# Optimization experiments

Measured on AMD Instinct MI355X. Metric: run time of the kernel, lower is better.

The kernel has to match this reference:

```python
import jax, jax.numpy as jnp
import numpy as np

NUM_CLASSES = 2
KS = 5  # kernel_size
EPS = 1e-8  # torch cosine_similarity eps


def setup_inputs() -> dict:
    key = jax.random.key(0)
    k1, k2, k3 = jax.random.split(key, 3)
    b, c, h, w = 8, 256, 128, 128
    er_input = jax.random.normal(k1, (b, c, h, w), dtype=jnp.float32)
    seg_label = jax.random.randint(k2, (b, h, w), 0, 2, dtype=jnp.int32)
    gt_boundary_seg = jax.random.randint(k3, (b, h, w), 0, 2, dtype=jnp.int32)
    return {"er_input": er_input, "seg_label": seg_label, "gt_boundary_seg": gt_boundary_seg}


def _context_loss(er_input, seg_label, gt_boundary_seg):
    # seg_label / gt_boundary_seg already at er_input spatial size (nearest interp is identity)
    b, c, h, w = er_input.shape
    r = KS // 2
    seg0 = jnp.where(seg_label == 255, 0, seg_label)
    gtb0 = jnp.where(gt_boundary_seg == 255, 0, gt_boundary_seg)
    gt_b = gtb0 * seg0                                  # [b,h,w] boundary pixels on fg classes
    interior = jnp.zeros((h, w), bool).at[r:h - r, r:w - r].set(True)
    valid = (gt_b > 0) & interior                       # pixels whose 5x5 window is in-bounds
    include = (gt_b > 0).any(axis=(1, 2))               # images contributing to scale_num
    cnt = valid.sum(axis=(1, 2)).astype(er_input.dtype)  # [b]

    norm = jnp.maximum(jnp.sqrt((er_input * er_input).sum(axis=1)), EPS)  # [b,h,w]
    validf = valid.astype(er_input.dtype)
    total = jnp.zeros((b,), dtype=er_input.dtype)
    n_shift = 0
    for dy in range(-r, r + 1):
        for dx in range(-r, r + 1):
            if dy == 0 and dx == 0:
                continue
            n_shift += 1
            # value at p+ (dy,dx) brought to p; valid pixels are interior so no wrap issue
            feat_s = jnp.roll(er_input, (-dy, -dx), axis=(2, 3))
            norm_s = jnp.roll(norm, (-dy, -dx), axis=(1, 2))
            seg_s = jnp.roll(seg_label, (-dy, -dx), axis=(1, 2))
            dot = (er_input * feat_s).sum(axis=1)       # [b,h,w]
            cos = dot / (norm * norm_s)
            # one_hot(seg,256)[:num_classes] dot product == labels equal AND label < num_classes
            labsim = ((seg_label == seg_s) & (seg_label < NUM_CLASSES)).astype(er_input.dtype)
            sq = (cos - labsim) ** 2
            # mse_loss over selected boundary pixels of image i
            total = total + (sq * validf).sum(axis=(1, 2)) / jnp.maximum(cnt, 1.0)
    loss_i = total / float(n_shift)                     # per-image context_loss_pi / 24
    scale_num = jnp.maximum(include.sum(), 1)
    return (loss_i * include.astype(loss_i.dtype)).sum() / scale_num.astype(loss_i.dtype)


def reference(er_input, seg_label, gt_boundary_seg):
    return _context_loss(er_input, seg_label, gt_boundary_seg)
```

## Files before the change

### kernel.cpp

```cpp
#include <hip/hip_runtime.h>
#include <math.h>

#define BATCH 8
#define CH    256
#define H     128
#define W     128
#define PLANE (H * W)
#define NPIX  (BATCH * PLANE)
#define NSHIFT 12
#define NMAPS  13
#define NCHUNK 4
#define CPC    (CH / NCHUNK)
#define CSTRIDE (NMAPS * NPIX)

static __device__ __constant__ int S_DY[NSHIFT] = {0,0,1,1,1,1,1,2,2,2,2,2};
static __device__ __constant__ int S_DX[NSHIFT] = {1,2,-2,-1,0,1,2,-2,-1,0,1,2};

#define TROWS  8
#define NTILE  (H / TROWS)
#define NCORRB (BATCH * NTILE * NCHUNK)
#define NSTATB (BATCH * 32)

__device__ __forceinline__ void fma4(float& acc, const float4& a, const float4& b) {
    acc = fmaf(a.x, b.x, acc);
    acc = fmaf(a.y, b.y, acc);
    acc = fmaf(a.z, b.z, acc);
    acc = fmaf(a.w, b.w, acc);
}

__global__ __launch_bounds__(64) void k_prep(int* __restrict__ cnt,
                                             int* __restrict__ inc,
                                             float* __restrict__ out) {
    int t = threadIdx.x;
    if (t < 8) { cnt[t] = 0; inc[t] = 0; }
    if (t == 0) out[0] = 0.0f;
}

__global__ __launch_bounds__(512, 4) void k_corr(const float* __restrict__ er,
                                                 const int* __restrict__ seg,
                                                 const int* __restrict__ gtb,
                                                 float* __restrict__ comb,
                                                 int* __restrict__ cnt,
                                                 int* __restrict__ inc) {
    __shared__ float4 lds[2][10][132];
    int t = threadIdx.x;

    if (blockIdx.x >= NCORRB) {
        int blk2 = blockIdx.x - NCORRB;
        int b = blk2 >> 5;
        int i = (blk2 & 31) * 512 + t;
        int my_cnt = 0, my_any = 0;
        {
            int s = seg[b * PLANE + i];
            int g = gtb[b * PLANE + i];
            int s0 = (s == 255) ? 0 : s;
            int g0 = (g == 255) ? 0 : g;
            if (s0 > 0 && g0 > 0) {
                my_any = 1;
                int y = i >> 7, x = i & 127;
                if (y >= 2 && y < H - 2 && x >= 2 && x < W - 2) my_cnt = 1;
            }
        }
        for (int o = 32; o > 0; o >>= 1) {
            my_cnt += __shfl_down(my_cnt, o, 64);
            my_any |= __shfl_down(my_any, o, 64);
        }
        __shared__ int sc[8], sa[8];
        int lane = t & 63, wid = t >> 6;
        if (lane == 0) { sc[wid] = my_cnt; sa[wid] = my_any; }
        __syncthreads();
        if (t == 0) {
            int c = 0, a = 0;
#pragma unroll
            for (int w2 = 0; w2 < 8; ++w2) { c += sc[w2]; a |= sa[w2]; }
            if (c) atomicAdd(&cnt[b], c);
            if (a) atomicOr(&inc[b], 1);
        }
        return;
    }

    int blk = blockIdx.x;
    int chunk = blk & 3;
    int tile  = (blk >> 2) & 15;
    int b     = blk >> 6;
    int y0 = tile * TROWS;
    int c0 = chunk * CPC;
    int r = t >> 7;
    int x = t & 127;

    if (t < 80) {
        int bi = t / 40, rem = t % 40;
        int row = rem >> 2, col = rem & 3;
        int xs = (col < 2) ? col : (col + 128);
        lds[bi][row][xs] = make_float4(0.f, 0.f, 0.f, 0.f);
    }

    float accA[13], accB[13];
#pragma unroll
    for (int i = 0; i < 13; i++) { accA[i] = 0.0f; accB[i] = 0.0f; }

    const float* base = er + (size_t)b * CH * PLANE;

    float pf[3][4];
    auto load_quad = [&](int c) {
#pragma unroll
        for (int k = 0; k < 3; ++k) {
            if (k < 2 || t < 256) {
                int s = t + k * 512;
                int row = s >> 7;
                int xs = s & 127;
                int y = y0 + row;
                if (y < H) {
                    const float* p0 = base + (size_t)c * PLANE + y * W + xs;
                    pf[k][0] = p0[0];
                    pf[k][1] = p0[PLANE];
                    pf[k][2] = p0[2 * PLANE];
                    pf[k][3] = p0[3 * PLANE];
                } else {
                    pf[k][0] = 0.f; pf[k][1] = 0.f; pf[k][2] = 0.f; pf[k][3] = 0.f;
                }
            }
        }
    };
    auto commit_quad = [&](int bi) {
#pragma unroll
        for (int k = 0; k < 3; ++k) {
            if (k < 2 || t < 256) {
                int s = t + k * 512;
                int row = s >> 7;
                int xs = s & 127;
                lds[bi][row][xs + 2] = make_float4(pf[k][0], pf[k][1], pf[k][2], pf[k][3]);
            }
        }
    };

    const int iters = CPC / 4;
    load_quad(c0);
    commit_quad(0);
    load_quad(c0 + 4);

    auto iter = [&](int it, int cur) {
        __syncthreads();
        if (it + 1 < iters) commit_quad(cur ^ 1);
        if (it + 2 < iters) load_quad(c0 + 4 * (it + 2));

        const float4* lp = &lds[cur][2 * r][x + 2];
        float4 cA = lp[0];
        float4 cB = lp[132];
        {
            float4 v1 = lp[1], v2 = lp[2];
            fma4(accA[0], cA, cA);
            fma4(accA[1], cA, v1);
            fma4(accA[2], cA, v2);
        }
        {
            float4 m2 = lp[130], m1 = lp[131], p1 = lp[133], p2 = lp[134];
            fma4(accA[3], cA, m2);
            fma4(accA[4], cA, m1);
            fma4(accA[5], cA, cB);
            fma4(accA[6], cA, p1);
            fma4(accA[7], cA, p2);
            fma4(accB[0], cB, cB);
            fma4(accB[1], cB, p1);
            fma4(accB[2], cB, p2);
        }
        {
            float4 m2 = lp[262], m1 = lp[263], v0 = lp[264], p1 = lp[265], p2 = lp[266];
            fma4(accA[8],  cA, m2);
            fma4(accA[9],  cA, m1);
            fma4(accA[10], cA, v0);
            fma4(accA[11], cA, p1);
            fma4(accA[12], cA, p2);
            fma4(accB[3], cB, m2);
            fma4(accB[4], cB, m1);
            fma4(accB[5], cB, v0);
            fma4(accB[6], cB, p1);
            fma4(accB[7], cB, p2);
        }
        {
            float4 m2 = lp[394], m1 = lp[395], v0 = lp[396], p1 = lp[397], p2 = lp[398];
            fma4(accB[8],  cB, m2);
            fma4(accB[9],  cB, m1);
            fma4(accB[10], cB, v0);
            fma4(accB[11], cB, p1);
            fma4(accB[12], cB, p2);
        }
    };

    for (int it = 0; it < iters; it += 2) {
        iter(it, 0);
        iter(it + 1, 1);
    }

    float* cb = comb + (size_t)chunk * CSTRIDE;
    int pixA = b * PLANE + (y0 + 2 * r) * W + x;
    int pixB = pixA + W;
#pragma unroll
    for (int m = 0; m < NSHIFT; ++m) {
        cb[m * NPIX + pixA] = accA[m + 1];
        cb[m * NPIX + pixB] = accB[m + 1];
    }
    cb[NSHIFT * NPIX + pixA] = accA[0];
    cb[NSHIFT * NPIX + pixB] = accB[0];
}

__global__ __launch_bounds__(256) void k_rn(const float* __restrict__ comb,
                                            float* __restrict__ rn) {
    int idx = blockIdx.x * 256 + threadIdx.x;
    const float* ns = comb + NSHIFT * NPIX;
    float s = (ns[idx] + ns[idx + CSTRIDE]) + (ns[idx + 2 * CSTRIDE] + ns[idx + 3 * CSTRIDE]);
    rn[idx] = fminf(rsqrtf(s), 1e8f);
}

__device__ __forceinline__ float sum4c(const float* __restrict__ p) {
    return (p[0] + p[CSTRIDE]) + (p[2 * CSTRIDE] + p[3 * CSTRIDE]);
}

__global__ __launch_bounds__(256) void k_loss(const float* __restrict__ comb,
                                              const float* __restrict__ rn,
                                              const int* __restrict__ seg,
                                              const int* __restrict__ gtb,
                                              const int* __restrict__ cnt,
                                              const int* __restrict__ inc,
                                              float* __restrict__ out) {
    const float* dots = comb;
    int idx = blockIdx.x * 256 + threadIdx.x;
    int b = idx >> 14;
    int rem = idx & (PLANE - 1);
    int y = rem >> 7;
    int x = rem & 127;

    int sn = 0;
#pragma unroll
    for (int b2 = 0; b2 < BATCH; b2++) sn += (inc[b2] != 0);
    if (sn < 1) sn = 1;
    int cb = cnt[b]; if (cb < 1) cb = 1;
    float factor = inc[b] ? 1.0f / (24.0f * (float)cb * (float)sn) : 0.0f;

    float val = 0.0f;
    if (y >= 2 && y < H - 2 && x >= 2 && x < W - 2) {
        int sp = seg[idx];
        int gp = gtb[idx];
        int s0 = (sp == 255) ? 0 : sp;
        int g0 = (gp == 255) ? 0 : gp;
        if (s0 > 0 && g0 > 0) {
            float npr = rn[idx];
            float sum = 0.0f;
#pragma unroll
            for (int i = 0; i < NSHIFT; ++i) {
                int off = S_DY[i] * W + S_DX[i];
                {
                    float d  = sum4c(dots + i * NPIX + idx);
                    float cosv = d * (npr * rn[idx + off]);
                    int sq = seg[idx + off];
                    float lab = (sp == sq && sp < 2) ? 1.0f : 0.0f;
                    float tt = cosv - lab;
                    sum = fmaf(tt, tt, sum);
                }
                {
                    float d  = sum4c(dots + i * NPIX + idx - off);
                    float cosv = d * (npr * rn[idx - off]);
                    int sq = seg[idx - off];
                    float lab = (sp == sq && sp < 2) ? 1.0f : 0.0f;
                    float tt = cosv - lab;
                    sum = fmaf(tt, tt, sum);
                }
            }
            val = sum * factor;
        }
    }

    for (int o = 32; o > 0; o >>= 1)
        val += __shfl_down(val, o, 64);
    __shared__ float wsum[4];
    int lane = threadIdx.x & 63;
    int wid  = threadIdx.x >> 6;
    if (lane == 0) wsum[wid] = val;
    __syncthreads();
    if (threadIdx.x == 0) {
        float s = wsum[0] + wsum[1] + wsum[2] + wsum[3];
        atomicAdd(out, s);
    }
}

extern "C" void kernel_launch(void* const* d_in, const int* in_sizes, int n_in,
                              void* d_out, int out_size, void* d_ws, size_t ws_size,
                              hipStream_t stream) {
    const float* er  = (const float*)d_in[0];
    const int*   seg = (const int*)d_in[1];
    const int*   gtb = (const int*)d_in[2];
    float* out = (float*)d_out;

    float* ws   = (float*)d_ws;
    float* comb = ws;
    float* rn   = comb + NCHUNK * CSTRIDE;
    int*   cnt  = (int*)(rn + NPIX);
    int*   inc  = cnt + 8;

    hipLaunchKernelGGL(k_prep, dim3(1), dim3(64), 0, stream, cnt, inc, out);
    hipLaunchKernelGGL(k_corr, dim3(NCORRB + NSTATB), dim3(512), 0, stream,
                       er, seg, gtb, comb, cnt, inc);
    hipLaunchKernelGGL(k_rn, dim3(NPIX / 256), dim3(256), 0, stream, comb, rn);
    hipLaunchKernelGGL(k_loss, dim3(NPIX / 256), dim3(256), 0, stream,
                       comb, rn, seg, gtb, cnt, inc, out);
}
```

Measured before the change: 215.7 us.

## Double correlation tile height and move label stats into loss kernel

The correlation kernel now processes 16-row tiles with 1024-thread blocks, so the 2-row halo is loaded relative to more output rows and the block count is halved. The per-image boundary count and include statistics move out of the correlation launch into the loss kernel's reduction. Per-image sums are accumulated atomically, and a new finalize kernel applies the normalisation. This cuts redundant halo traffic and removes the extra stat blocks, but it adds a kernel launch. Larger blocks with a 4-blocks-per-CU launch bound may also limit registers for the 26 accumulators and reduce occupancy or grid fill (256 blocks).

Result: slower. 223.4 us (+3.6%).

```diff
diff --git a/kernel.cpp b/kernel.cpp
--- a/kernel.cpp
+++ b/kernel.cpp
@@ -16,10 +16,10 @@
 static __device__ __constant__ int S_DY[NSHIFT] = {0,0,1,1,1,1,1,2,2,2,2,2};
 static __device__ __constant__ int S_DX[NSHIFT] = {1,2,-2,-1,0,1,2,-2,-1,0,1,2};
 
-#define TROWS  8
+#define TROWS  16
+#define SROWS  (TROWS + 2)
 #define NTILE  (H / TROWS)
 #define NCORRB (BATCH * NTILE * NCHUNK)
-#define NSTATB (BATCH * 32)
 
 __device__ __forceinline__ void fma4(float& acc, const float4& a, const float4& b) {
     acc = fmaf(a.x, b.x, acc);
@@ -30,66 +30,27 @@
 
 __global__ __launch_bounds__(64) void k_prep(int* __restrict__ cnt,
                                              int* __restrict__ inc,
-                                             float* __restrict__ out) {
+                                             float* __restrict__ tot) {
     int t = threadIdx.x;
-    if (t < 8) { cnt[t] = 0; inc[t] = 0; }
-    if (t == 0) out[0] = 0.0f;
-}
-
-__global__ __launch_bounds__(512, 4) void k_corr(const float* __restrict__ er,
-                                                 const int* __restrict__ seg,
-                                                 const int* __restrict__ gtb,
-                                                 float* __restrict__ comb,
-                                                 int* __restrict__ cnt,
-                                                 int* __restrict__ inc) {
-    __shared__ float4 lds[2][10][132];
+    if (t < 8) { cnt[t] = 0; inc[t] = 0; tot[t] = 0.0f; }
+}
+
+__global__ __launch_bounds__(1024, 4) void k_corr(const float* __restrict__ er,
+                                                  float* __restrict__ comb) {
+    __shared__ float4 lds[2][SROWS][132];
     int t = threadIdx.x;
-
-    if (blockIdx.x >= NCORRB) {
-        int blk2 = blockIdx.x - NCORRB;
-        int b = blk2 >> 5;
-        int i = (blk2 & 31) * 512 + t;
-        int my_cnt = 0, my_any = 0;
-        {
-            int s = seg[b * PLANE + i];
-            int g = gtb[b * PLANE + i];
-            int s0 = (s == 255) ? 0 : s;
-            int g0 = (g == 255) ? 0 : g;
-            if (s0 > 0 && g0 > 0) {
-                my_any = 1;
-                int y = i >> 7, x = i & 127;
-                if (y >= 2 && y < H - 2 && x >= 2 && x < W - 2) my_cnt = 1;
-            }
-        }
-        for (int o = 32; o > 0; o >>= 1) {
-            my_cnt += __shfl_down(my_cnt, o, 64);
-            my_any |= __shfl_down(my_any, o, 64);
-        }
-        __shared__ int sc[8], sa[8];
-        int lane = t & 63, wid = t >> 6;
-        if (lane == 0) { sc[wid] = my_cnt; sa[wid] = my_any; }
-        __syncthreads();
-        if (t == 0) {
-            int c = 0, a = 0;
-#pragma unroll
-            for (int w2 = 0; w2 < 8; ++w2) { c += sc[w2]; a |= sa[w2]; }
-            if (c) atomicAdd(&cnt[b], c);
-            if (a) atomicOr(&inc[b], 1);
-        }
-        return;
-    }
 
     int blk = blockIdx.x;
     int chunk = blk & 3;
-    int tile  = (blk >> 2) & 15;
-    int b     = blk >> 6;
+    int tile  = (blk >> 2) & 7;
+    int b     = blk >> 5;
     int y0 = tile * TROWS;
     int c0 = chunk * CPC;
     int r = t >> 7;
     int x = t & 127;
 
-    if (t < 80) {
-        int bi = t / 40, rem = t % 40;
+    if (t < 2 * SROWS * 4) {
+        int bi = t / (SROWS * 4), rem = t % (SROWS * 4);
         int row = rem >> 2, col = rem & 3;
         int xs = (col < 2) ? col : (col + 128);
         lds[bi][row][xs] = make_float4(0.f, 0.f, 0.f, 0.f);
@@ -106,7 +67,7 @@
 #pragma unroll
         for (int k = 0; k < 3; ++k) {
             if (k < 2 || t < 256) {
-                int s = t + k * 512;
+                int s = t + k * 1024;
                 int row = s >> 7;
                 int xs = s & 127;
                 int y = y0 + row;
@@ -126,7 +87,7 @@
 #pragma unroll
         for (int k = 0; k < 3; ++k) {
             if (k < 2 || t < 256) {
-                int s = t + k * 512;
+                int s = t + k * 1024;
                 int row = s >> 7;
                 int xs = s & 127;
                 lds[bi][row][xs + 2] = make_float4(pf[k][0], pf[k][1], pf[k][2], pf[k][3]);
@@ -220,9 +181,9 @@
                                               const float* __restrict__ rn,
                                               const int* __restrict__ seg,
                                               const int* __restrict__ gtb,
-                                              const int* __restrict__ cnt,
-                                              const int* __restrict__ inc,
-                                              float* __restrict__ out) {
+                                              int* __restrict__ cnt,
+                                              int* __restrict__ inc,
+                                              float* __restrict__ tot) {
     const float* dots = comb;
     int idx = blockIdx.x * 256 + threadIdx.x;
     int b = idx >> 14;
@@ -230,56 +191,81 @@
     int y = rem >> 7;
     int x = rem & 127;
 
-    int sn = 0;
-#pragma unroll
-    for (int b2 = 0; b2 < BATCH; b2++) sn += (inc[b2] != 0);
-    if (sn < 1) sn = 1;
-    int cb = cnt[b]; if (cb < 1) cb = 1;
-    float factor = inc[b] ? 1.0f / (24.0f * (float)cb * (float)sn) : 0.0f;
-
     float val = 0.0f;
-    if (y >= 2 && y < H - 2 && x >= 2 && x < W - 2) {
+    int my_cnt = 0, my_any = 0;
+    {
         int sp = seg[idx];
         int gp = gtb[idx];
         int s0 = (sp == 255) ? 0 : sp;
         int g0 = (gp == 255) ? 0 : gp;
         if (s0 > 0 && g0 > 0) {
-            float npr = rn[idx];
-            float sum = 0.0f;
-#pragma unroll
-            for (int i = 0; i < NSHIFT; ++i) {
-                int off = S_DY[i] * W + S_DX[i];
-                {
-                    float d  = sum4c(dots + i * NPIX + idx);
-                    float cosv = d * (npr * rn[idx + off]);
-                    int sq = seg[idx + off];
-                    float lab = (sp == sq && sp < 2) ? 1.0f : 0.0f;
-                    float tt = cosv - lab;
-                    sum = fmaf(tt, tt, sum);
+            my_any = 1;
+            if (y >= 2 && y < H - 2 && x >= 2 && x < W - 2) {
+                my_cnt = 1;
+                float npr = rn[idx];
+                float sum = 0.0f;
+#pragma unroll
+                for (int i = 0; i < NSHIFT; ++i) {
+                    int off = S_DY[i] * W + S_DX[i];
+                    {
+                        float d  = sum4c(dots + i * NPIX + idx);
+                        float cosv = d * (npr * rn[idx + off]);
+                        int sq = seg[idx + off];
+                        float lab = (sp == sq && sp < 2) ? 1.0f : 0.0f;
+                        float tt = cosv - lab;
+                        sum = fmaf(tt, tt, sum);
+                    }
+                    {
+                        float d  = sum4c(dots + i * NPIX + idx - off);
+                        float cosv = d * (npr * rn[idx - off]);
+                        int sq = seg[idx - off];
+                        float lab = (sp == sq && sp < 2) ? 1.0f : 0.0f;
+                        float tt = cosv - lab;
+                        sum = fmaf(tt, tt, sum);
+                    }
                 }
-                {
-                    float d  = sum4c(dots + i * NPIX + idx - off);
-                    float cosv = d * (npr * rn[idx - off]);
-                    int sq = seg[idx - off];
-                    float lab = (sp == sq && sp < 2) ? 1.0f : 0.0f;
-                    float tt = cosv - lab;
-                    sum = fmaf(tt, tt, sum);
-                }
+                val = sum;
             }
-            val = sum * factor;
-        }
-    }
-
-    for (int o = 32; o > 0; o >>= 1)
-        val += __shfl_down(val, o, 64);
+        }
+    }
+
+    for (int o = 32; o > 0; o >>= 1) {
+        val    += __shfl_down(val, o, 64);
+        my_cnt += __shfl_down(my_cnt, o, 64);
+        my_any |= __shfl_down(my_any, o, 64);
+    }
     __shared__ float wsum[4];
+    __shared__ int wc[4], wa[4];
     int lane = threadIdx.x & 63;
     int wid  = threadIdx.x >> 6;
-    if (lane == 0) wsum[wid] = val;
+    if (lane == 0) { wsum[wid] = val; wc[wid] = my_cnt; wa[wid] = my_any; }
     __syncthreads();
     if (threadIdx.x == 0) {
         float s = wsum[0] + wsum[1] + wsum[2] + wsum[3];
-        atomicAdd(out, s);
+        int c = wc[0] + wc[1] + wc[2] + wc[3];
+        int a = wa[0] | wa[1] | wa[2] | wa[3];
+        if (s != 0.0f) atomicAdd(&tot[b], s);
+        if (c) atomicAdd(&cnt[b], c);
+        if (a) atomicOr(&inc[b], 1);
+    }
+}
+
+__global__ __launch_bounds__(64) void k_fin(const int* __restrict__ cnt,
+                                            const int* __restrict__ inc,
+                                            const float* __restrict__ tot,
+                                            float* __restrict__ out) {
+    if (threadIdx.x == 0) {
+        int sn = 0;
+        float s = 0.0f;
+#pragma unroll
+        for (int b = 0; b < BATCH; ++b) {
+            int ib = inc[b];
+            sn += (ib != 0);
+            int cb = cnt[b]; if (cb < 1) cb = 1;
+            if (ib) s += tot[b] / (24.0f * (float)cb);
+        }
+        if (sn < 1) sn = 1;
+        out[0] = s / (float)sn;
     }
 }
 
@@ -294,13 +280,14 @@
     float* ws   = (float*)d_ws;
     float* comb = ws;
     float* rn   = comb + NCHUNK * CSTRIDE;
-    int*   cnt  = (int*)(rn + NPIX);
+    float* tot  = rn + NPIX;
+    int*   cnt  = (int*)(tot + 8);
     int*   inc  = cnt + 8;
 
-    hipLaunchKernelGGL(k_prep, dim3(1), dim3(64), 0, stream, cnt, inc, out);
-    hipLaunchKernelGGL(k_corr, dim3(NCORRB + NSTATB), dim3(512), 0, stream,
-                       er, seg, gtb, comb, cnt, inc);
+    hipLaunchKernelGGL(k_prep, dim3(1), dim3(64), 0, stream, cnt, inc, tot);
+    hipLaunchKernelGGL(k_corr, dim3(NCORRB), dim3(1024), 0, stream, er, comb);
     hipLaunchKernelGGL(k_rn, dim3(NPIX / 256), dim3(256), 0, stream, comb, rn);
     hipLaunchKernelGGL(k_loss, dim3(NPIX / 256), dim3(256), 0, stream,
-                       comb, rn, seg, gtb, cnt, inc, out);
-}
+                       comb, rn, seg, gtb, cnt, inc, tot);
+    hipLaunchKernelGGL(k_fin, dim3(1), dim3(64), 0, stream, cnt, inc, tot, out);
+}
```
